# Performance work log

Hardware: AMD Instinct MI355X
Metric: run time of the kernel (lower is better)

The kernel has to match this reference:

```python
import jax, jax.numpy as jnp
import numpy as np

D, NH, L, P, FF = 256, 8, 3, 4, 1024
DH = D // NH
EPS = 1e-5

def _ln(x, g, b):
    m = jnp.mean(x, axis=-1, keepdims=True)
    v = jnp.mean((x - m) ** 2, axis=-1, keepdims=True)
    return (x - m) * jax.lax.rsqrt(v + EPS) * g + b

def _bilinear(value, loc, Hl, Wl):
    # value: [B,NH,Nl,DH]; loc (x,y) in [0,1]: [B,N,NH,P,2]; grid_sample align_corners=False, zero padding
    B, N = loc.shape[0], loc.shape[1]
    x = loc[..., 0] * Wl - 0.5
    y = loc[..., 1] * Hl - 0.5
    x0 = jnp.floor(x)
    y0 = jnp.floor(y)
    lx, ly = x - x0, y - y0
    x0 = x0.astype(jnp.int32)
    y0 = y0.astype(jnp.int32)

    def gather(xi, yi):
        valid = ((xi >= 0) & (xi < Wl) & (yi >= 0) & (yi < Hl)).astype(value.dtype)
        idx = jnp.clip(yi, 0, Hl - 1) * Wl + jnp.clip(xi, 0, Wl - 1)  # [B,N,NH,P]
        idx = idx.transpose(0, 2, 1, 3).reshape(B, NH, N * P, 1)
        v = jnp.take_along_axis(value, idx, axis=2)  # [B,NH,N*P,DH]
        v = v.reshape(B, NH, N, P, DH).transpose(0, 2, 1, 3, 4)  # [B,N,NH,P,DH]
        return v * valid[..., None]

    v00 = gather(x0, y0)
    v01 = gather(x0 + 1, y0)
    v10 = gather(x0, y0 + 1)
    v11 = gather(x0 + 1, y0 + 1)
    return (v00 * ((1 - lx) * (1 - ly))[..., None] + v01 * (lx * (1 - ly))[..., None]
            + v10 * ((1 - lx) * ly)[..., None] + v11 * (lx * ly)[..., None])

def _forward(query, p3, p4, p5, Wv, bv, Woff, boff, Wattn, battn, Wref, bref, Wo, bo,
             W1, b1, W2, b2, g1, be1, g2, be2, shapes):
    B, N, _ = query.shape
    off = (query @ Woff + boff).reshape(B, N, NH, L, P, 2)
    aw = jax.nn.softmax((query @ Wattn + battn).reshape(B, N, NH, L * P), axis=-1).reshape(B, N, NH, L, P)
    ref = jax.nn.sigmoid(query @ Wref + bref)[:, :, None, None, :]  # [B,N,1,1,2]
    out = jnp.zeros((B, N, NH, DH), query.dtype)
    for l, (feat, (Hl, Wl)) in enumerate(zip((p3, p4, p5), shapes)):
        val = (feat @ Wv + bv).reshape(B, Hl * Wl, NH, DH).transpose(0, 2, 1, 3)  # [B,NH,Nl,DH]
        loc = ref + off[:, :, :, l] / jnp.array([Wl, Hl], query.dtype)  # offsets normalized by (W,H)
        samp = _bilinear(val, loc, Hl, Wl)  # [B,N,NH,P,DH]
        out = out + jnp.einsum('bnhp,bnhpd->bnhd', aw[:, :, :, l], samp)
    attn_out = out.reshape(B, N, D) @ Wo + bo
    q = _ln(query + attn_out, g1, be1)  # residual + norm1 (dropout=eval identity)
    ffn = jax.nn.gelu(q @ W1 + b1, approximate=False) @ W2 + b2
    return _ln(q + ffn, g2, be2)

def setup_inputs():
    key = jax.random.key(0)
    ks = jax.random.split(key, 12)
    B = 4
    H3, W3, H4, W4, H5, W5 = 100, 100, 50, 50, 25, 25
    N = H3 * W3 + H4 * W4 + H5 * W5
    s = 0.02
    f32 = jnp.float32
    return dict(
        query=jax.random.normal(ks[0], (B, N, D), f32),
        p3=jax.random.normal(ks[1], (B, H3 * W3, D), f32),
        p4=jax.random.normal(ks[2], (B, H4 * W4, D), f32),
        p5=jax.random.normal(ks[3], (B, H5 * W5, D), f32),
        Wv=jax.random.normal(ks[4], (D, D), f32) * s, bv=jnp.zeros((D,), f32),
        Woff=jax.random.normal(ks[5], (D, NH * L * P * 2), f32) * s, boff=jnp.zeros((NH * L * P * 2,), f32),
        Wattn=jax.random.normal(ks[6], (D, NH * L * P), f32) * s, battn=jnp.zeros((NH * L * P,), f32),
        Wref=jax.random.normal(ks[7], (D, 2), f32) * s, bref=jnp.zeros((2,), f32),
        Wo=jax.random.normal(ks[8], (D, D), f32) * s, bo=jnp.zeros((D,), f32),
        W1=jax.random.normal(ks[9], (D, FF), f32) * s, b1=jnp.zeros((FF,), f32),
        W2=jax.random.normal(ks[10], (FF, D), f32) * s, b2=jnp.zeros((D,), f32),
        g1=jnp.ones((D,), f32), be1=jnp.zeros((D,), f32),
        g2=jnp.ones((D,), f32), be2=jnp.zeros((D,), f32),
        H3=H3, W3=W3, H4=H4, W4=W4, H5=H5, W5=W5,
    )

def reference(query, p3, p4, p5, Wv, bv, Woff, boff, Wattn, battn, Wref, bref, Wo, bo,
              W1, b1, W2, b2, g1, be1, g2, be2, H3, W3, H4, W4, H5, W5):
    return _forward(query, p3, p4, p5, Wv, bv, Woff, boff, Wattn, battn, Wref, bref, Wo, bo,
                    W1, b1, W2, b2, g1, be1, g2, be2, ((H3, W3), (H4, W4), (H5, W5)))
```

## Files before the change

kernel.cpp:

```cpp
#include <hip/hip_runtime.h>
#include <math.h>

#define BQ    4
#define NTOT  13125
#define DD    256
#define NHH   8
#define FFD   1024
#define EPSLN 1e-5f
#define MROWS (BQ * NTOT)
#define MPAD  52736

typedef __bf16 bf16_t;
typedef bf16_t bf16x8 __attribute__((ext_vector_type(8)));
typedef float floatx4 __attribute__((ext_vector_type(4)));

__device__ __forceinline__ unsigned short f2bf(float f) {
    unsigned u = __float_as_uint(f);
    return (unsigned short)((u + 0x7FFFu + ((u >> 16) & 1u)) >> 16);
}
__device__ __forceinline__ float bf2f(unsigned short h) {
    return __uint_as_float(((unsigned)h) << 16);
}

typedef const __attribute__((address_space(1))) unsigned int* gptr_t;
typedef __attribute__((address_space(3))) unsigned int* lptr_t;
__device__ __forceinline__ void gld16(const void* g, void* l) {
    __builtin_amdgcn_global_load_lds((gptr_t)g, (lptr_t)l, 16, 0, 0);
}

enum { EPI_F32 = 0, EPI_GELU = 2, EPI_VALSEG = 3 };

__device__ __forceinline__ int val_row(int gm) {
    if (gm < 40064) {
        if (gm >= 40000) return -1;
        int b = gm / 10000; int nl = gm - b * 10000;
        return b * NTOT + nl;
    } else if (gm < 50176) {
        int r = gm - 40064;
        if (r >= 10000) return -1;
        int b = r / 2500; int nl = r - b * 2500;
        return b * NTOT + 10000 + nl;
    } else {
        int r = gm - 50176;
        if (r >= 2500) return -1;
        int b = r / 625; int nl = r - b * 625;
        return b * NTOT + 12500 + nl;
    }
}

template <int EPI, typename OutT>
__launch_bounds__(256)
__global__ void mm_k(const unsigned short* __restrict__ A,
                     const unsigned short* __restrict__ Bt,
                     const float* __restrict__ bias, OutT* __restrict__ C,
                     int M, int K, int Nout, int ldc, int Mstore) {
    __shared__ __align__(16) unsigned short As[128 * 32];
    __shared__ __align__(16) unsigned short Bs[128 * 32];

    const int tid = threadIdx.x;
    const int m0 = blockIdx.x * 128;
    const int n0 = blockIdx.y * 128;
    const int w = tid >> 6, lane = tid & 63;
    const int q = lane >> 4, l15 = lane & 15;
    const int wm = (w & 1) * 64, wn = (w >> 1) * 64;

    const int sr = tid >> 2;
    const int sk = (tid & 3) * 8;

    const unsigned short* Ag = A + (size_t)(m0 + sr) * K + sk;
    const unsigned short* Bg = Bt + (size_t)(n0 + sr) * K + sk;
    char* AsB = (char*)As;
    char* BsB = (char*)Bs;

    floatx4 acc[4][4];
#pragma unroll
    for (int t = 0; t < 4; t++)
#pragma unroll
        for (int u = 0; u < 4; u++) {
            floatx4 z = {0.f, 0.f, 0.f, 0.f};
            acc[t][u] = z;
        }

    for (int k0 = 0; k0 < K; k0 += 32) {
        gld16(Ag + k0, AsB + tid * 16);
        gld16(Ag + (size_t)64 * K + k0, AsB + 4096 + tid * 16);
        gld16(Bg + k0, BsB + tid * 16);
        gld16(Bg + (size_t)64 * K + k0, BsB + 4096 + tid * 16);
        __syncthreads();

        bf16x8 af[4], bfr[4];
#pragma unroll
        for (int t = 0; t < 4; t++)
            af[t] = *reinterpret_cast<const bf16x8*>(&As[(wm + t * 16 + l15) * 32 + q * 8]);
#pragma unroll
        for (int u = 0; u < 4; u++)
            bfr[u] = *reinterpret_cast<const bf16x8*>(&Bs[(wn + u * 16 + l15) * 32 + q * 8]);
#pragma unroll
        for (int t = 0; t < 4; t++)
#pragma unroll
            for (int u = 0; u < 4; u++)
                acc[t][u] = __builtin_amdgcn_mfma_f32_16x16x32_bf16(af[t], bfr[u], acc[t][u], 0, 0, 0);
        __syncthreads();
    }

    float bias_v[4];
#pragma unroll
    for (int u = 0; u < 4; u++) {
        int gn = n0 + wn + u * 16 + l15;
        bias_v[u] = (gn < Nout) ? bias[gn] : 0.f;
    }

#pragma unroll
    for (int t = 0; t < 4; t++) {
#pragma unroll
        for (int r = 0; r < 4; r++) {
            int gm = m0 + wm + t * 16 + q * 4 + r;
            int orow = gm;
            if (EPI == EPI_VALSEG) orow = val_row(gm);
#pragma unroll
            for (int u = 0; u < 4; u++) {
                int gn = n0 + wn + u * 16 + l15;
                if (gn >= Nout) continue;
                float v = acc[t][u][r] + bias_v[u];
                if (EPI == EPI_GELU) {
                    v = 0.5f * v * (1.f + erff(v * 0.70710678118f));
                    if (gm < Mstore) {
                        float ov = (gm < M) ? v : 0.f;
                        ((unsigned short*)C)[(size_t)gm * ldc + gn] = f2bf(ov);
                    }
                } else if (EPI == EPI_VALSEG) {
                    if (orow >= 0)
                        ((unsigned short*)C)[(size_t)orow * ldc + gn] = f2bf(v);
                } else {
                    if (gm < M) ((float*)C)[(size_t)gm * ldc + gn] = v;
                }
            }
        }
    }
}

template <typename RT, typename OT>
__launch_bounds__(256)
__global__ void gemmln_k(const unsigned short* __restrict__ A,
                         const unsigned short* __restrict__ Bt,
                         const float* __restrict__ bias, const RT* __restrict__ res,
                         const float* __restrict__ g, const float* __restrict__ be,
                         OT* __restrict__ out, int M, int K) {
    __shared__ __align__(16) unsigned short As[64 * 32];
    __shared__ __align__(16) unsigned short Bs[256 * 32];

    const int tid = threadIdx.x;
    const int m0 = blockIdx.x * 64;
    const int w = tid >> 6, lane = tid & 63;
    const int q = lane >> 4, l15 = lane & 15;
    const int wn = w * 64;

    const int sr = tid >> 2;
    const int sk = (tid & 3) * 8;
    const unsigned short* Ag = A + (size_t)(m0 + sr) * K + sk;
    const unsigned short* Bg = Bt + (size_t)sr * K + sk;
    char* AsB = (char*)As;
    char* BsB = (char*)Bs;

    floatx4 acc[4][4];
#pragma unroll
    for (int t = 0; t < 4; t++)
#pragma unroll
        for (int u = 0; u < 4; u++) {
            floatx4 z = {0.f, 0.f, 0.f, 0.f};
            acc[t][u] = z;
        }

    for (int k0 = 0; k0 < K; k0 += 32) {
        gld16(Ag + k0, AsB + tid * 16);
#pragma unroll
        for (int j = 0; j < 4; j++)
            gld16(Bg + (size_t)j * 64 * K + k0, BsB + j * 4096 + tid * 16);
        __syncthreads();

        bf16x8 af[4], bfr[4];
#pragma unroll
        for (int t = 0; t < 4; t++)
            af[t] = *reinterpret_cast<const bf16x8*>(&As[(t * 16 + l15) * 32 + q * 8]);
#pragma unroll
        for (int u = 0; u < 4; u++)
            bfr[u] = *reinterpret_cast<const bf16x8*>(&Bs[(wn + u * 16 + l15) * 32 + q * 8]);
#pragma unroll
        for (int t = 0; t < 4; t++)
#pragma unroll
            for (int u = 0; u < 4; u++)
                acc[t][u] = __builtin_amdgcn_mfma_f32_16x16x32_bf16(af[t], bfr[u], acc[t][u], 0, 0, 0);
        __syncthreads();
    }

    float gg[4], bb[4], bias_v[4];
#pragma unroll
    for (int u = 0; u < 4; u++) {
        int gn = wn + u * 16 + l15;
        gg[u] = g[gn]; bb[u] = be[gn]; bias_v[u] = bias[gn];
    }

    float x[4][4][4];
    float ssum[4][4], ssq[4][4];
#pragma unroll
    for (int t = 0; t < 4; t++) {
#pragma unroll
        for (int r = 0; r < 4; r++) {
            int gm = m0 + t * 16 + q * 4 + r;
            bool valid = gm < M;
            float s = 0.f, sq = 0.f;
#pragma unroll
            for (int u = 0; u < 4; u++) {
                int gn = wn + u * 16 + l15;
                float rv = 0.f;
                if (valid) {
                    if (sizeof(RT) == 2)
                        rv = bf2f(((const unsigned short*)res)[(size_t)gm * DD + gn]);
                    else
                        rv = ((const float*)res)[(size_t)gm * DD + gn];
                }
                float xx = acc[t][u][r] + bias_v[u] + rv;
                x[t][r][u] = xx;
                s += xx; sq += xx * xx;
            }
            ssum[t][r] = s; ssq[t][r] = sq;
        }
    }
#pragma unroll
    for (int m = 1; m <= 8; m <<= 1) {
#pragma unroll
        for (int t = 0; t < 4; t++)
#pragma unroll
            for (int r = 0; r < 4; r++) {
                ssum[t][r] += __shfl_xor(ssum[t][r], m);
                ssq[t][r] += __shfl_xor(ssq[t][r], m);
            }
    }
    float* Ls = (float*)As;
    float* Lq = Ls + 256;
    if (l15 == 0) {
#pragma unroll
        for (int t = 0; t < 4; t++)
#pragma unroll
            for (int r = 0; r < 4; r++) {
                int lr = t * 16 + q * 4 + r;
                Ls[lr * 4 + w] = ssum[t][r];
                Lq[lr * 4 + w] = ssq[t][r];
            }
    }
    __syncthreads();

#pragma unroll
    for (int t = 0; t < 4; t++) {
#pragma unroll
        for (int r = 0; r < 4; r++) {
            int lr = t * 16 + q * 4 + r;
            int gm = m0 + lr;
            float tot = Ls[lr * 4 + 0] + Ls[lr * 4 + 1] + Ls[lr * 4 + 2] + Ls[lr * 4 + 3];
            float totq = Lq[lr * 4 + 0] + Lq[lr * 4 + 1] + Lq[lr * 4 + 2] + Lq[lr * 4 + 3];
            float mean = tot * (1.f / DD);
            float var = totq * (1.f / DD) - mean * mean;
            float rs = rsqrtf(var + EPSLN);
            if (gm < M) {
#pragma unroll
                for (int u = 0; u < 4; u++) {
                    int gn = wn + u * 16 + l15;
                    float o = (x[t][r][u] - mean) * rs * gg[u] + bb[u];
                    if (sizeof(OT) == 2)
                        ((unsigned short*)out)[(size_t)gm * DD + gn] = f2bf(o);
                    else
                        ((float*)out)[(size_t)gm * DD + gn] = o;
                }
            }
        }
    }
}

__launch_bounds__(256)
__global__ void ffn_k(const unsigned short* __restrict__ A,
                      const unsigned short* __restrict__ Wt1,
                      const float* __restrict__ b1,
                      const unsigned short* __restrict__ Wt2,
                      const float* __restrict__ b2,
                      const float* __restrict__ g, const float* __restrict__ be,
                      float* __restrict__ out, int M) {
    __shared__ __align__(16) unsigned short qs[8 * 64 * 32];
    __shared__ __align__(16) unsigned short Hs[64 * 128];

    const int tid = threadIdx.x;
    const int m0 = blockIdx.x * 64;
    const int w = tid >> 6, lane = tid & 63;
    const int q = lane >> 4, l15 = lane & 15;
    const int wn1 = w * 32;
    const int wn2 = w * 64;

    {
        const int sr = tid >> 2;
        const int sk = (tid & 3) * 8;
        const unsigned short* Ag = A + (size_t)(m0 + sr) * 256 + sk;
        char* qsB = (char*)qs;
#pragma unroll
        for (int p = 0; p < 8; p++)
            gld16(Ag + p * 32, qsB + p * 4096 + tid * 16);
    }

    floatx4 acc2[4][4];
#pragma unroll
    for (int t = 0; t < 4; t++)
#pragma unroll
        for (int u = 0; u < 4; u++) {
            floatx4 z = {0.f, 0.f, 0.f, 0.f};
            acc2[t][u] = z;
        }

    __syncthreads();

#pragma unroll 1
    for (int j = 0; j < 8; j++) {
        floatx4 acc1[4][2];
#pragma unroll
        for (int t = 0; t < 4; t++)
#pragma unroll
            for (int u2 = 0; u2 < 2; u2++) {
                floatx4 z = {0.f, 0.f, 0.f, 0.f};
                acc1[t][u2] = z;
            }
        const unsigned short* W1p = Wt1 + (size_t)(j * 128 + wn1) * 256;
#pragma unroll
        for (int kk = 0; kk < 8; kk++) {
            bf16x8 af[4], bf1[2];
#pragma unroll
            for (int t = 0; t < 4; t++)
                af[t] = *reinterpret_cast<const bf16x8*>(&qs[kk * 2048 + (t * 16 + l15) * 32 + q * 8]);
#pragma unroll
            for (int u2 = 0; u2 < 2; u2++)
                bf1[u2] = *reinterpret_cast<const bf16x8*>(&W1p[(size_t)(u2 * 16 + l15) * 256 + kk * 32 + q * 8]);
#pragma unroll
            for (int t = 0; t < 4; t++)
#pragma unroll
                for (int u2 = 0; u2 < 2; u2++)
                    acc1[t][u2] = __builtin_amdgcn_mfma_f32_16x16x32_bf16(af[t], bf1[u2], acc1[t][u2], 0, 0, 0);
        }
        __syncthreads();
#pragma unroll
        for (int u2 = 0; u2 < 2; u2++) {
            int col = wn1 + u2 * 16 + l15;
            float bv = b1[j * 128 + col];
#pragma unroll
            for (int t = 0; t < 4; t++)
#pragma unroll
                for (int r = 0; r < 4; r++) {
                    int row = t * 16 + q * 4 + r;
                    float v = acc1[t][u2][r] + bv;
                    v = 0.5f * v * (1.f + erff(v * 0.70710678118f));
                    int bo = (row * 256 + col * 2) ^ ((row & 7) << 4);
                    *(unsigned short*)((char*)Hs + bo) = f2bf(v);
                }
        }
        __syncthreads();
        const unsigned short* W2p = Wt2 + (size_t)wn2 * 1024 + j * 128;
#pragma unroll
        for (int kk2 = 0; kk2 < 4; kk2++) {
            bf16x8 af2[4], bf2[4];
#pragma unroll
            for (int t = 0; t < 4; t++) {
                int row = t * 16 + l15;
                int bo = (row * 256 + (kk2 * 32 + q * 8) * 2) ^ ((row & 7) << 4);
                af2[t] = *reinterpret_cast<const bf16x8*>((const char*)Hs + bo);
            }
#pragma unroll
            for (int u = 0; u < 4; u++)
                bf2[u] = *reinterpret_cast<const bf16x8*>(&W2p[(size_t)(u * 16 + l15) * 1024 + kk2 * 32 + q * 8]);
#pragma unroll
            for (int t = 0; t < 4; t++)
#pragma unroll
                for (int u = 0; u < 4; u++)
                    acc2[t][u] = __builtin_amdgcn_mfma_f32_16x16x32_bf16(af2[t], bf2[u], acc2[t][u], 0, 0, 0);
        }
    }

    float gg[4], bb[4], bias_v[4];
#pragma unroll
    for (int u = 0; u < 4; u++) {
        int gn = wn2 + u * 16 + l15;
        gg[u] = g[gn]; bb[u] = be[gn]; bias_v[u] = b2[gn];
    }

    float x[4][4][4];
    float ssum[4][4], ssq[4][4];
#pragma unroll
    for (int t = 0; t < 4; t++) {
#pragma unroll
        for (int r = 0; r < 4; r++) {
            int row = t * 16 + q * 4 + r;
            float s = 0.f, sq = 0.f;
#pragma unroll
            for (int u = 0; u < 4; u++) {
                int gn = wn2 + u * 16 + l15;
                float rv = bf2f(qs[(gn >> 5) * 2048 + row * 32 + (gn & 31)]);
                float xx = acc2[t][u][r] + bias_v[u] + rv;
                x[t][r][u] = xx;
                s += xx; sq += xx * xx;
            }
            ssum[t][r] = s; ssq[t][r] = sq;
        }
    }
#pragma unroll
    for (int m = 1; m <= 8; m <<= 1) {
#pragma unroll
        for (int t = 0; t < 4; t++)
#pragma unroll
            for (int r = 0; r < 4; r++) {
                ssum[t][r] += __shfl_xor(ssum[t][r], m);
                ssq[t][r] += __shfl_xor(ssq[t][r], m);
            }
    }
    __syncthreads();
    float* Ls = (float*)qs;
    float* Lq = Ls + 256;
    if (l15 == 0) {
#pragma unroll
        for (int t = 0; t < 4; t++)
#pragma unroll
            for (int r = 0; r < 4; r++) {
                int lr = t * 16 + q * 4 + r;
                Ls[lr * 4 + w] = ssum[t][r];
                Lq[lr * 4 + w] = ssq[t][r];
            }
    }
    __syncthreads();

#pragma unroll
    for (int t = 0; t < 4; t++) {
#pragma unroll
        for (int r = 0; r < 4; r++) {
            int lr = t * 16 + q * 4 + r;
            int gm = m0 + lr;
            float tot = Ls[lr * 4 + 0] + Ls[lr * 4 + 1] + Ls[lr * 4 + 2] + Ls[lr * 4 + 3];
            float totq = Lq[lr * 4 + 0] + Lq[lr * 4 + 1] + Lq[lr * 4 + 2] + Lq[lr * 4 + 3];
            float mean = tot * (1.f / DD);
            float var = totq * (1.f / DD) - mean * mean;
            float rs = rsqrtf(var + EPSLN);
            if (gm < M) {
#pragma unroll
                for (int u = 0; u < 4; u++) {
                    int gn = wn2 + u * 16 + l15;
                    out[(size_t)gm * DD + gn] = (x[t][r][u] - mean) * rs * gg[u] + bb[u];
                }
            }
        }
    }
}

#define QELEMS   13500416
#define F3ELEMS  10256384
#define F4ELEMS   2588672
#define TOTELEMS 27000832

__launch_bounds__(256)
__global__ void cast_acts_k(const float* __restrict__ query, const float* __restrict__ p3,
                            const float* __restrict__ p4, const float* __restrict__ p5,
                            unsigned short* __restrict__ qbf, unsigned short* __restrict__ featsb) {
    int idx4 = (blockIdx.x * 256 + threadIdx.x) * 4;
    if (idx4 >= TOTELEMS) return;
    const float* src; unsigned short* dst; int local, real;
    if (idx4 < QELEMS) {
        src = query; dst = qbf; local = idx4; real = 13440000;
    } else {
        int j = idx4 - QELEMS;
        if (j < F3ELEMS)              { src = p3; dst = featsb;                    local = j;            real = 10240000; }
        else if (j < F3ELEMS + F4ELEMS){ src = p4; dst = featsb + F3ELEMS;         local = j - F3ELEMS;  real = 2560000; }
        else                          { src = p5; dst = featsb + F3ELEMS + F4ELEMS; local = j - F3ELEMS - F4ELEMS; real = 640000; }
    }
    float4 v = make_float4(0.f, 0.f, 0.f, 0.f);
    if (local < real) v = *(const float4*)&src[local];
    ushort4 o;
    o.x = f2bf(v.x); o.y = f2bf(v.y); o.z = f2bf(v.z); o.w = f2bf(v.w);
    *(ushort4*)&dst[local] = o;
}

#define WTQ_E   98304
#define WTV_E   (WTQ_E + 65536)
#define WTO_E   (WTV_E + 65536)
#define WT1_E   (WTO_E + 262144)
#define WT2_E   (WT1_E + 262144)
#define PREP_TOT (WT2_E + 384)

__launch_bounds__(256)
__global__ void prep_w_k(const float* __restrict__ Woff, const float* __restrict__ Wattn,
                         const float* __restrict__ Wref, const float* __restrict__ Wv,
                         const float* __restrict__ Wo, const float* __restrict__ W1,
                         const float* __restrict__ W2, const float* __restrict__ boff,
                         const float* __restrict__ battn, const float* __restrict__ bref,
                         unsigned short* __restrict__ warena, float* __restrict__ biasq) {
    int i = blockIdx.x * 256 + threadIdx.x;
    if (i >= PREP_TOT) return;
    if (i >= WT2_E) {
        int t = i - WT2_E;
        biasq[t] = (t < 192) ? boff[t] : (t < 288 ? battn[t - 192] : (t < 290 ? bref[t - 288] : 0.f));
        return;
    }
    float v;
    if (i < WTQ_E) {
        int n = i >> 8, k = i & 255;
        v = (n < 192) ? Woff[k * 192 + n]
          : (n < 288) ? Wattn[k * 96 + (n - 192)]
          : (n < 290) ? Wref[k * 2 + (n - 288)] : 0.f;
    } else if (i < WTV_E) {
        int j = i - WTQ_E; int n = j >> 8, k = j & 255;
        v = Wv[k * 256 + n];
    } else if (i < WTO_E) {
        int j = i - WTV_E; int n = j >> 8, k = j & 255;
        v = Wo[k * 256 + n];
    } else if (i < WT1_E) {
        int j = i - WTO_E; int n = j >> 8, k = j & 255;
        v = W1[k * 1024 + n];
    } else {
        int j = i - WT1_E; int n = j >> 10, k = j & 1023;
        v = W2[k * 256 + n];
    }
    warena[i] = f2bf(v);
}

__launch_bounds__(256)
__global__ void softmax12_k(const float* __restrict__ projb, unsigned short* __restrict__ aw) {
    int rh = blockIdx.x * 256 + threadIdx.x;
    if (rh >= MROWS * NHH) return;
    int bn = rh >> 3, h = rh & 7;
    const float* p = projb + (size_t)bn * 320 + 192 + h * 12;
    float v[12], mx = -1e30f;
#pragma unroll
    for (int i = 0; i < 12; i++) { v[i] = p[i]; mx = fmaxf(mx, v[i]); }
    float s = 0.f;
#pragma unroll
    for (int i = 0; i < 12; i++) { v[i] = expf(v[i] - mx); s += v[i]; }
    float inv = 1.f / s;
    unsigned short* o = aw + (size_t)rh * 12;
#pragma unroll
    for (int i = 0; i < 12; i++) o[i] = f2bf(v[i] * inv);
}

__launch_bounds__(128)
__global__ void sample_k(const unsigned short* __restrict__ val, const float* __restrict__ projb,
                         const unsigned short* __restrict__ aw,
                         unsigned short* __restrict__ out) {
    const int wv = threadIdx.x >> 6;
    const int lane = threadIdx.x & 63;
    const int bn = blockIdx.x * 2 + wv;
    const int b = bn / NTOT;
    __shared__ uint2 sc[2][96][4];

    const float* prow = projb + (size_t)bn * 320;
    float rx = 1.f / (1.f + expf(-prow[288]));
    float ry = 1.f / (1.f + expf(-prow[289]));
    for (int s0 = lane; s0 < 96; s0 += 64) {
        const int lp = s0 % 12;
        const int l = lp >> 2;
        int Hl, Wl, loff;
        if (l == 0)      { Hl = 100; Wl = 100; loff = 0; }
        else if (l == 1) { Hl = 50;  Wl = 50;  loff = 10000; }
        else             { Hl = 25;  Wl = 25;  loff = 12500; }
        float ox = prow[s0 * 2 + 0];
        float oy = prow[s0 * 2 + 1];
        float a  = bf2f(aw[(size_t)bn * 96 + s0]);
        float x = rx * (float)Wl + ox - 0.5f;
        float y = ry * (float)Hl + oy - 0.5f;
        x = fminf(fmaxf(x, -1e4f), 1e4f);
        y = fminf(fmaxf(y, -1e4f), 1e4f);
        float x0f = floorf(x), y0f = floorf(y);
        float lx = x - x0f, ly = y - y0f;
        int x0 = (int)x0f, y0 = (int)y0f;
#pragma unroll
        for (int c = 0; c < 4; c++) {
            int xi = x0 + (c & 1);
            int yi = y0 + (c >> 1);
            bool ok = (xi >= 0) && (xi < Wl) && (yi >= 0) && (yi < Hl);
            int xc = min(max(xi, 0), Wl - 1);
            int yc = min(max(yi, 0), Hl - 1);
            int idx = b * NTOT + loff + yc * Wl + xc;
            float wgt = ((c & 1) ? lx : 1.f - lx) * ((c >> 1) ? ly : 1.f - ly);
            sc[wv][s0][c] = make_uint2(__float_as_uint(ok ? a * wgt : 0.f), (unsigned)(idx * 512));
        }
    }
    __syncthreads();

    const int h = lane >> 3;
    const int dq = (lane & 7) * 4;
    const char* vb = (const char*)val + h * 64 + dq * 2;
    float a0 = 0.f, a1 = 0.f, a2 = 0.f, a3 = 0.f;
#pragma unroll
    for (int lp = 0; lp < 12; lp++) {
        int s = h * 12 + lp;
#pragma unroll
        for (int c = 0; c < 4; c++) {
            uint2 p = sc[wv][s][c];
            float wgt = __uint_as_float(p.x);
            uint2 u = *(const uint2*)(vb + p.y);
            a0 += wgt * __uint_as_float(u.x << 16);
            a1 += wgt * __uint_as_float(u.x & 0xFFFF0000u);
            a2 += wgt * __uint_as_float(u.y << 16);
            a3 += wgt * __uint_as_float(u.y & 0xFFFF0000u);
        }
    }
    uint2 ov;
    ov.x = (unsigned)f2bf(a0) | ((unsigned)f2bf(a1) << 16);
    ov.y = (unsigned)f2bf(a2) | ((unsigned)f2bf(a3) << 16);
    *(uint2*)(out + (size_t)bn * DD + h * 32 + dq) = ov;
}

extern "C" void kernel_launch(void* const* d_in, const int* in_sizes, int n_in,
                              void* d_out, int out_size, void* d_ws, size_t ws_size,
                              hipStream_t stream) {
    const float* query = (const float*)d_in[0];
    const float* p3    = (const float*)d_in[1];
    const float* p4    = (const float*)d_in[2];
    const float* p5    = (const float*)d_in[3];
    const float* Wv    = (const float*)d_in[4];
    const float* bv    = (const float*)d_in[5];
    const float* Woff  = (const float*)d_in[6];
    const float* boff  = (const float*)d_in[7];
    const float* Wattn = (const float*)d_in[8];
    const float* battn = (const float*)d_in[9];
    const float* Wref  = (const float*)d_in[10];
    const float* bref  = (const float*)d_in[11];
    const float* Wo    = (const float*)d_in[12];
    const float* bo    = (const float*)d_in[13];
    const float* W1    = (const float*)d_in[14];
    const float* b1    = (const float*)d_in[15];
    const float* W2    = (const float*)d_in[16];
    const float* b2    = (const float*)d_in[17];
    const float* g1    = (const float*)d_in[18];
    const float* be1   = (const float*)d_in[19];
    const float* g2    = (const float*)d_in[20];
    const float* be2   = (const float*)d_in[21];
    float* outp = (float*)d_out;

    char* wsb = (char*)d_ws;
    unsigned short* qbf    = (unsigned short*)(wsb + 0);
    float*          projb  = (float*)(wsb + 27000832);
    unsigned short* awb    = (unsigned short*)(wsb + 94502912);
    unsigned short* featsb = (unsigned short*)(wsb + 104582912);
    unsigned short* valb   = (unsigned short*)(wsb + 131583744);
    unsigned short* sampb  = (unsigned short*)(wsb + 158463744);
    unsigned short* warena = (unsigned short*)(wsb + 185399296);
    float*          biasq  = (float*)(wsb + 186906624);

    unsigned short* Wtq = warena;
    unsigned short* Wtv = warena + WTQ_E;
    unsigned short* Wto = warena + WTV_E;
    unsigned short* Wt1 = warena + WTO_E;
    unsigned short* Wt2 = warena + WT1_E;

    cast_acts_k<<<dim3(TOTELEMS / 4 / 256), 256, 0, stream>>>(query, p3, p4, p5, qbf, featsb);
    prep_w_k<<<dim3((PREP_TOT + 255) / 256), 256, 0, stream>>>(
        Woff, Wattn, Wref, Wv, Wo, W1, W2, boff, battn, bref, warena, biasq);
    mm_k<EPI_F32, float><<<dim3(MPAD / 128, 3), 256, 0, stream>>>(
        qbf, Wtq, biasq, projb, MROWS, 256, 290, 320, 0);
    softmax12_k<<<dim3((MROWS * NHH + 255) / 256), 256, 0, stream>>>(projb, awb);
    mm_k<EPI_VALSEG, unsigned short><<<dim3(MPAD / 128, 2), 256, 0, stream>>>(
        featsb, Wtv, bv, valb, 0, 256, 256, 256, 0);
    sample_k<<<dim3(MROWS / 2), 128, 0, stream>>>(valb, projb, awb, sampb);
    gemmln_k<float, unsigned short><<<dim3((MROWS + 63) / 64), 256, 0, stream>>>(
        sampb, Wto, bo, query, g1, be1, qbf, MROWS, 256);
    ffn_k<<<dim3((MROWS + 63) / 64), 256, 0, stream>>>(
        qbf, Wt1, b1, Wt2, b2, g2, be2, outp, MROWS);
}
```

Measured before the change: 565.1 us.

## Split FFN kernel across 8 waves per block instead of 4

The fused FFN kernel now runs 512 threads (8 waves) per 64-row block. Each wave computes half as many output columns in both GEMMs, which halves its accumulator registers, and the LayerNorm partial sums are reduced across 8 waves. The aim is more waves in flight per CU to hide global weight-load latency. The cost is more block barriers contending and smaller per-wave MFMA tiles with less register reuse of the A fragments.

```diff
diff --git a/kernel.cpp b/kernel.cpp
--- a/kernel.cpp
+++ b/kernel.cpp
@@ -276,7 +276,7 @@
     }
 }
 
-__launch_bounds__(256)
+__launch_bounds__(512, 4)
 __global__ void ffn_k(const unsigned short* __restrict__ A,
                       const unsigned short* __restrict__ Wt1,
                       const float* __restrict__ b1,
@@ -291,24 +291,25 @@
     const int m0 = blockIdx.x * 64;
     const int w = tid >> 6, lane = tid & 63;
     const int q = lane >> 4, l15 = lane & 15;
-    const int wn1 = w * 32;
-    const int wn2 = w * 64;
 
     {
-        const int sr = tid >> 2;
-        const int sk = (tid & 3) * 8;
-        const unsigned short* Ag = A + (size_t)(m0 + sr) * 256 + sk;
         char* qsB = (char*)qs;
 #pragma unroll
-        for (int p = 0; p < 8; p++)
-            gld16(Ag + p * 32, qsB + p * 4096 + tid * 16);
-    }
-
-    floatx4 acc2[4][4];
+        for (int p = 0; p < 4; p++) {
+            int idx = p * 8 + w;
+            int kkb = idx >> 2;
+            int row = (idx & 3) * 16 + (lane >> 2);
+            int c = lane & 3;
+            gld16(A + (size_t)(m0 + row) * 256 + kkb * 32 + c * 8,
+                  qsB + idx * 1024 + lane * 16);
+        }
+    }
+
+    floatx4 acc2[4][2];
 #pragma unroll
     for (int t = 0; t < 4; t++)
 #pragma unroll
-        for (int u = 0; u < 4; u++) {
+        for (int u = 0; u < 2; u++) {
             floatx4 z = {0.f, 0.f, 0.f, 0.f};
             acc2[t][u] = z;
         }
@@ -317,51 +318,44 @@
 
 #pragma unroll 1
     for (int j = 0; j < 8; j++) {
-        floatx4 acc1[4][2];
-#pragma unroll
-        for (int t = 0; t < 4; t++)
-#pragma unroll
-            for (int u2 = 0; u2 < 2; u2++) {
-                floatx4 z = {0.f, 0.f, 0.f, 0.f};
-                acc1[t][u2] = z;
-            }
-        const unsigned short* W1p = Wt1 + (size_t)(j * 128 + wn1) * 256;
+        floatx4 acc1[4];
+#pragma unroll
+        for (int t = 0; t < 4; t++) {
+            floatx4 z = {0.f, 0.f, 0.f, 0.f};
+            acc1[t] = z;
+        }
+        const unsigned short* W1p = Wt1 + (size_t)(j * 128 + w * 16 + l15) * 256;
 #pragma unroll
         for (int kk = 0; kk < 8; kk++) {
-            bf16x8 af[4], bf1[2];
+            bf16x8 af[4], bf1;
 #pragma unroll
             for (int t = 0; t < 4; t++)
                 af[t] = *reinterpret_cast<const bf16x8*>(&qs[kk * 2048 + (t * 16 + l15) * 32 + q * 8]);
-#pragma unroll
-            for (int u2 = 0; u2 < 2; u2++)
-                bf1[u2] = *reinterpret_cast<const bf16x8*>(&W1p[(size_t)(u2 * 16 + l15) * 256 + kk * 32 + q * 8]);
+            bf1 = *reinterpret_cast<const bf16x8*>(&W1p[kk * 32 + q * 8]);
 #pragma unroll
             for (int t = 0; t < 4; t++)
-#pragma unroll
-                for (int u2 = 0; u2 < 2; u2++)
-                    acc1[t][u2] = __builtin_amdgcn_mfma_f32_16x16x32_bf16(af[t], bf1[u2], acc1[t][u2], 0, 0, 0);
+                acc1[t] = __builtin_amdgcn_mfma_f32_16x16x32_bf16(af[t], bf1, acc1[t], 0, 0, 0);
         }
         __syncthreads();
-#pragma unroll
-        for (int u2 = 0; u2 < 2; u2++) {
-            int col = wn1 + u2 * 16 + l15;
+        {
+            int col = w * 16 + l15;
             float bv = b1[j * 128 + col];
 #pragma unroll
             for (int t = 0; t < 4; t++)
 #pragma unroll
                 for (int r = 0; r < 4; r++) {
                     int row = t * 16 + q * 4 + r;
-                    float v = acc1[t][u2][r] + bv;
+                    float v = acc1[t][r] + bv;
                     v = 0.5f * v * (1.f + erff(v * 0.70710678118f));
                     int bo = (row * 256 + col * 2) ^ ((row & 7) << 4);
                     *(unsigned short*)((char*)Hs + bo) = f2bf(v);
                 }
         }
         __syncthreads();
-        const unsigned short* W2p = Wt2 + (size_t)wn2 * 1024 + j * 128;
+        const unsigned short* W2p = Wt2 + (size_t)(w * 32) * 1024 + j * 128;
 #pragma unroll
         for (int kk2 = 0; kk2 < 4; kk2++) {
-            bf16x8 af2[4], bf2[4];
+            bf16x8 af2[4], bf2[2];
 #pragma unroll
             for (int t = 0; t < 4; t++) {
                 int row = t * 16 + l15;
@@ -369,24 +363,25 @@
                 af2[t] = *reinterpret_cast<const bf16x8*>((const char*)Hs + bo);
             }
 #pragma unroll
-            for (int u = 0; u < 4; u++)
+            for (int u = 0; u < 2; u++)
                 bf2[u] = *reinterpret_cast<const bf16x8*>(&W2p[(size_t)(u * 16 + l15) * 1024 + kk2 * 32 + q * 8]);
 #pragma unroll
             for (int t = 0; t < 4; t++)
 #pragma unroll
-                for (int u = 0; u < 4; u++)
+                for (int u = 0; u < 2; u++)
                     acc2[t][u] = __builtin_amdgcn_mfma_f32_16x16x32_bf16(af2[t], bf2[u], acc2[t][u], 0, 0, 0);
         }
     }
 
-    float gg[4], bb[4], bias_v[4];
-#pragma unroll
-    for (int u = 0; u < 4; u++) {
+    const int wn2 = w * 32;
+    float gg[2], bb[2], bias_v[2];
+#pragma unroll
+    for (int u = 0; u < 2; u++) {
         int gn = wn2 + u * 16 + l15;
         gg[u] = g[gn]; bb[u] = be[gn]; bias_v[u] = b2[gn];
     }
 
-    float x[4][4][4];
+    float x[4][4][2];
     float ssum[4][4], ssq[4][4];
 #pragma unroll
     for (int t = 0; t < 4; t++) {
@@ -395,7 +390,7 @@
             int row = t * 16 + q * 4 + r;
             float s = 0.f, sq = 0.f;
 #pragma unroll
-            for (int u = 0; u < 4; u++) {
+            for (int u = 0; u < 2; u++) {
                 int gn = wn2 + u * 16 + l15;
                 float rv = bf2f(qs[(gn >> 5) * 2048 + row * 32 + (gn & 31)]);
                 float xx = acc2[t][u][r] + bias_v[u] + rv;
@@ -417,15 +412,15 @@
     }
     __syncthreads();
     float* Ls = (float*)qs;
-    float* Lq = Ls + 256;
+    float* Lq = Ls + 512;
     if (l15 == 0) {
 #pragma unroll
         for (int t = 0; t < 4; t++)
 #pragma unroll
             for (int r = 0; r < 4; r++) {
                 int lr = t * 16 + q * 4 + r;
-                Ls[lr * 4 + w] = ssum[t][r];
-                Lq[lr * 4 + w] = ssq[t][r];
+                Ls[lr * 8 + w] = ssum[t][r];
+                Lq[lr * 8 + w] = ssq[t][r];
             }
     }
     __syncthreads();
@@ -436,14 +431,18 @@
         for (int r = 0; r < 4; r++) {
             int lr = t * 16 + q * 4 + r;
             int gm = m0 + lr;
-            float tot = Ls[lr * 4 + 0] + Ls[lr * 4 + 1] + Ls[lr * 4 + 2] + Ls[lr * 4 + 3];
-            float totq = Lq[lr * 4 + 0] + Lq[lr * 4 + 1] + Lq[lr * 4 + 2] + Lq[lr * 4 + 3];
+            float tot = 0.f, totq = 0.f;
+#pragma unroll
+            for (int ww = 0; ww < 8; ww++) {
+                tot += Ls[lr * 8 + ww];
+                totq += Lq[lr * 8 + ww];
+            }
             float mean = tot * (1.f / DD);
             float var = totq * (1.f / DD) - mean * mean;
             float rs = rsqrtf(var + EPSLN);
             if (gm < M) {
 #pragma unroll
-                for (int u = 0; u < 4; u++) {
+                for (int u = 0; u < 2; u++) {
                     int gn = wn2 + u * 16 + l15;
                     out[(size_t)gm * DD + gn] = (x[t][r][u] - mean) * rs * gg[u] + bb[u];
                 }
@@ -662,6 +661,6 @@
     sample_k<<<dim3(MROWS / 2), 128, 0, stream>>>(valb, projb, awb, sampb);
     gemmln_k<float, unsigned short><<<dim3((MROWS + 63) / 64), 256, 0, stream>>>(
         sampb, Wto, bo, query, g1, be1, qbf, MROWS, 256);
-    ffn_k<<<dim3((MROWS + 63) / 64), 256, 0, stream>>>(
+    ffn_k<<<dim3((MROWS + 63) / 64), 512, 0, stream>>>(
         qbf, Wt1, b1, Wt2, b2, g2, be2, outp, MROWS);
 }
```

After: 553.0 us, median of 2. -2.1%, faster.
